# Optimization experiments

Hardware: AMD Instinct MI355X
Metric: run time of the kernel (lower is better)

The kernel has to match this reference:

```python
import jax, jax.numpy as jnp
import numpy as np

B, T, S, D = 32, 128, 2048, 1024


def setup_inputs() -> dict:
    key = jax.random.key(0)
    k1, k2, k3, k4 = jax.random.split(key, 4)
    source = jax.random.normal(k1, (B, T, D), dtype=jnp.float32)
    memory_bank = jax.random.normal(k2, (B, S, D), dtype=jnp.float32)
    # lengths in [1, S] so no query row is fully masked
    memory_lengths = jax.random.randint(k3, (B,), 1, S + 1, dtype=jnp.int64)
    # nn.Linear(2*dim, dim, bias=False) weight, torch layout [out, in]
    bound = 1.0 / np.sqrt(2 * D)
    W_out = jax.random.uniform(k4, (D, 2 * D), dtype=jnp.float32, minval=-bound, maxval=bound)
    return {"source": source, "memory_bank": memory_bank,
            "W_out": W_out, "memory_lengths": memory_lengths}


def reference(source, memory_bank, W_out, memory_lengths):
    # dot score: [B, T, S]
    align = jnp.einsum("btd,bsd->bts", source, memory_bank)
    # sequence mask from lengths: [B, S]
    mask = jnp.arange(S)[None, :] < memory_lengths[:, None]
    align = jnp.where(mask[:, None, :], align, -jnp.inf)
    align_vectors = jax.nn.softmax(align, axis=-1)            # [B, T, S]
    c = jnp.einsum("bts,bsd->btd", align_vectors, memory_bank)  # [B, T, D]
    concat_c = jnp.concatenate([c, source], axis=-1)            # [B, T, 2D]
    attn_h = jnp.tanh(concat_c @ W_out.T)                       # [B, T, D]
    # transpose to [T, B, ...] as original (one_step=False path)
    return attn_h.transpose(1, 0, 2), align_vectors.transpose(1, 0, 2)
```

## Files before the change

### kernel.cpp

```cpp
#include <hip/hip_runtime.h>
#include <hip/hip_bf16.h>
#include <stdint.h>

#define B_ 32
#define T_ 128
#define S_ 2048
#define D_ 1024

typedef float floatx4 __attribute__((ext_vector_type(4)));
typedef float f32x4 __attribute__((ext_vector_type(4)));
typedef unsigned short u16x4 __attribute__((ext_vector_type(4)));
typedef unsigned short u16x8 __attribute__((ext_vector_type(8)));
typedef __bf16 bf16x8 __attribute__((ext_vector_type(8)));

__device__ __forceinline__ unsigned short f2bf(float x){
  __hip_bfloat16 h = __float2bfloat16(x);
  return __builtin_bit_cast(unsigned short, h);
}
__device__ __forceinline__ float bf2f(unsigned short u){
  __hip_bfloat16 h = __builtin_bit_cast(__hip_bfloat16, u);
  return __bfloat162float(h);
}
__device__ __forceinline__ f32x4 mfma16(u16x8 a, u16x8 b, f32x4 c){
  return __builtin_amdgcn_mfma_f32_16x16x32_bf16(
      __builtin_bit_cast(bf16x8, a), __builtin_bit_cast(bf16x8, b), c, 0, 0, 0);
}

__global__ __launch_bounds__(512, 4) void k_align(
    const float* __restrict__ src, const float* __restrict__ mb,
    float* __restrict__ logits)
{
  __shared__ unsigned short SH[2][4][128][32];
  const int b = blockIdx.x, sblk = blockIdx.y;
  const int tid = threadIdx.x, lane = tid & 63, wave = tid >> 6;
  const int wr = wave >> 2, wc = wave & 3;
  const float* Ag = src + (size_t)b * T_ * D_;
  const float* Bg = mb + (size_t)b * S_ * D_ + (size_t)sblk * 128 * D_;

  f32x4 acc[4][2];
  #pragma unroll
  for (int m = 0; m < 4; m++)
    #pragma unroll
    for (int n = 0; n < 2; n++) acc[m][n] = (f32x4){0.f, 0.f, 0.f, 0.f};

  const int r0 = tid >> 3;
  const int c40 = (tid & 7) * 4;
  const int sw0 = ((((c40 >> 3) ^ ((r0 >> 1) & 3)) << 3) | (c40 & 7));
  const int r1 = r0 + 64;
  const int sw1 = ((((c40 >> 3) ^ ((r1 >> 1) & 3)) << 3) | (c40 & 7));

  floatx4 ra[2], rb[2];
  ra[0] = *(const floatx4*)(Ag + (size_t)r0 * D_ + c40);
  ra[1] = *(const floatx4*)(Ag + (size_t)r1 * D_ + c40);
  rb[0] = *(const floatx4*)(Bg + (size_t)r0 * D_ + c40);
  rb[1] = *(const floatx4*)(Bg + (size_t)r1 * D_ + c40);

  {
    u16x4 ah, al, bh, bl;
    #pragma unroll
    for (int i = 0; i < 4; i++) {
      unsigned short h = f2bf(ra[0][i]); float hf = bf2f(h);
      ah[i] = h; al[i] = f2bf(ra[0][i] - hf);
      h = f2bf(rb[0][i]); hf = bf2f(h);
      bh[i] = h; bl[i] = f2bf(rb[0][i] - hf);
    }
    *(u16x4*)&SH[0][0][r0][sw0] = ah;
    *(u16x4*)&SH[0][1][r0][sw0] = al;
    *(u16x4*)&SH[0][2][r0][sw0] = bh;
    *(u16x4*)&SH[0][3][r0][sw0] = bl;
    #pragma unroll
    for (int i = 0; i < 4; i++) {
      unsigned short h = f2bf(ra[1][i]); float hf = bf2f(h);
      ah[i] = h; al[i] = f2bf(ra[1][i] - hf);
      h = f2bf(rb[1][i]); hf = bf2f(h);
      bh[i] = h; bl[i] = f2bf(rb[1][i] - hf);
    }
    *(u16x4*)&SH[0][0][r1][sw1] = ah;
    *(u16x4*)&SH[0][1][r1][sw1] = al;
    *(u16x4*)&SH[0][2][r1][sw1] = bh;
    *(u16x4*)&SH[0][3][r1][sw1] = bl;
  }
  __syncthreads();

  for (int it = 0; it < 32; ++it) {
    const int cur = it & 1, nxt = cur ^ 1;
    const bool more = (it + 1 < 32);
    if (more) {
      const int k0 = (it + 1) * 32;
      ra[0] = *(const floatx4*)(Ag + (size_t)r0 * D_ + k0 + c40);
      ra[1] = *(const floatx4*)(Ag + (size_t)r1 * D_ + k0 + c40);
      rb[0] = *(const floatx4*)(Bg + (size_t)r0 * D_ + k0 + c40);
      rb[1] = *(const floatx4*)(Bg + (size_t)r1 * D_ + k0 + c40);
    }
    {
      const int kb = (lane >> 4) << 3;
      u16x8 a_h[4], a_l[4], b_h[2], b_l[2];
      #pragma unroll
      for (int m = 0; m < 4; m++) {
        int r = wr * 64 + m * 16 + (lane & 15);
        int kbs = (((kb >> 3) ^ ((r >> 1) & 3)) << 3);
        a_h[m] = *(const u16x8*)&SH[cur][0][r][kbs];
        a_l[m] = *(const u16x8*)&SH[cur][1][r][kbs];
      }
      #pragma unroll
      for (int n = 0; n < 2; n++) {
        int r = wc * 32 + n * 16 + (lane & 15);
        int kbs = (((kb >> 3) ^ ((r >> 1) & 3)) << 3);
        b_h[n] = *(const u16x8*)&SH[cur][2][r][kbs];
        b_l[n] = *(const u16x8*)&SH[cur][3][r][kbs];
      }
      #pragma unroll
      for (int m = 0; m < 4; m++)
        #pragma unroll
        for (int n = 0; n < 2; n++) {
          acc[m][n] = mfma16(a_h[m], b_h[n], acc[m][n]);
          acc[m][n] = mfma16(a_h[m], b_l[n], acc[m][n]);
          acc[m][n] = mfma16(a_l[m], b_h[n], acc[m][n]);
        }
    }
    if (more) {
      u16x4 ah, al, bh, bl;
      #pragma unroll
      for (int i = 0; i < 4; i++) {
        unsigned short h = f2bf(ra[0][i]); float hf = bf2f(h);
        ah[i] = h; al[i] = f2bf(ra[0][i] - hf);
        h = f2bf(rb[0][i]); hf = bf2f(h);
        bh[i] = h; bl[i] = f2bf(rb[0][i] - hf);
      }
      *(u16x4*)&SH[nxt][0][r0][sw0] = ah;
      *(u16x4*)&SH[nxt][1][r0][sw0] = al;
      *(u16x4*)&SH[nxt][2][r0][sw0] = bh;
      *(u16x4*)&SH[nxt][3][r0][sw0] = bl;
      #pragma unroll
      for (int i = 0; i < 4; i++) {
        unsigned short h = f2bf(ra[1][i]); float hf = bf2f(h);
        ah[i] = h; al[i] = f2bf(ra[1][i] - hf);
        h = f2bf(rb[1][i]); hf = bf2f(h);
        bh[i] = h; bl[i] = f2bf(rb[1][i] - hf);
      }
      *(u16x4*)&SH[nxt][0][r1][sw1] = ah;
      *(u16x4*)&SH[nxt][1][r1][sw1] = al;
      *(u16x4*)&SH[nxt][2][r1][sw1] = bh;
      *(u16x4*)&SH[nxt][3][r1][sw1] = bl;
    }
    __syncthreads();
  }

  #pragma unroll
  for (int m = 0; m < 4; m++)
    #pragma unroll
    for (int n = 0; n < 2; n++)
      #pragma unroll
      for (int j = 0; j < 4; j++) {
        int t = wr * 64 + m * 16 + ((lane >> 4) << 2) + j;
        int s = sblk * 128 + wc * 32 + n * 16 + (lane & 15);
        logits[((size_t)b * T_ + t) * S_ + s] = acc[m][n][j];
      }
}

__global__ __launch_bounds__(256) void k_softmax(
    const float* __restrict__ logits, const int* __restrict__ lens,
    float* __restrict__ out1, unsigned short* __restrict__ pbf)
{
  const int bt = blockIdx.x;
  const int b = bt >> 7, t = bt & 127;
  const int probe = lens[1];
  const int len = (probe == 0) ? lens[2 * b] : lens[b];
  const float* row = logits + (size_t)bt * S_;
  const int tid = threadIdx.x, lane = tid & 63, wave = tid >> 6;

  floatx4 v[2];
  float mx = -3.0e38f;
  #pragma unroll
  for (int j = 0; j < 2; j++) {
    int f4 = tid + 256 * j;
    v[j] = *(const floatx4*)(row + f4 * 4);
    #pragma unroll
    for (int i = 0; i < 4; i++) {
      int s = f4 * 4 + i;
      if (s < len) mx = fmaxf(mx, v[j][i]);
    }
  }
  #pragma unroll
  for (int off = 1; off < 64; off <<= 1) mx = fmaxf(mx, __shfl_xor(mx, off));
  __shared__ float red[8];
  if (lane == 0) red[wave] = mx;
  __syncthreads();
  mx = fmaxf(fmaxf(red[0], red[1]), fmaxf(red[2], red[3]));

  float sum = 0.f;
  floatx4 e[2];
  #pragma unroll
  for (int j = 0; j < 2; j++) {
    int f4 = tid + 256 * j;
    #pragma unroll
    for (int i = 0; i < 4; i++) {
      int s = f4 * 4 + i;
      float ee = (s < len) ? __expf(v[j][i] - mx) : 0.f;
      e[j][i] = ee; sum += ee;
    }
  }
  #pragma unroll
  for (int off = 1; off < 64; off <<= 1) sum += __shfl_xor(sum, off);
  if (lane == 0) red[4 + wave] = sum;
  __syncthreads();
  sum = red[4] + red[5] + red[6] + red[7];
  const float inv = 1.0f / sum;

  float* orow = out1 + ((size_t)t * B_ + b) * S_;
  unsigned short* prow = pbf + (size_t)bt * S_;
  #pragma unroll
  for (int j = 0; j < 2; j++) {
    int f4 = tid + 256 * j;
    floatx4 o;
    u16x4 pk;
    #pragma unroll
    for (int i = 0; i < 4; i++) { o[i] = e[j][i] * inv; pk[i] = f2bf(o[i]); }
    *(floatx4*)(orow + f4 * 4) = o;
    *(u16x4*)(prow + f4 * 4) = pk;
  }
}

__global__ __launch_bounds__(256, 2) void k_pv(
    const unsigned short* __restrict__ pbf, const float* __restrict__ mb,
    float* __restrict__ cout)
{
  __shared__ unsigned short As[128][72];
  __shared__ unsigned short BsT[64][72];
  const int b = blockIdx.x, dblk = blockIdx.y;
  const int tid = threadIdx.x, lane = tid & 63, wave = tid >> 6;
  const int wr = wave >> 1, wc = wave & 1;
  const unsigned short* Pg = pbf + (size_t)b * T_ * S_;
  const float* Bg = mb + (size_t)b * S_ * D_ + dblk * 64;

  f32x4 acc[4][2];
  #pragma unroll
  for (int m = 0; m < 4; m++)
    #pragma unroll
    for (int n = 0; n < 2; n++) acc[m][n] = (f32x4){0.f, 0.f, 0.f, 0.f};

  const int gs = tid & 15, gd = tid >> 4;
  const int s0 = gs * 4, d0 = gd * 4;

  u16x8 ra[4];
  floatx4 rb[4];
  #pragma unroll
  for (int j = 0; j < 4; j++) {
    int g = tid + 256 * j;
    int row = g >> 3, c8 = (g & 7) * 8;
    ra[j] = *(const u16x8*)(Pg + (size_t)row * S_ + c8);
  }
  #pragma unroll
  for (int j = 0; j < 4; j++)
    rb[j] = *(const floatx4*)(Bg + (size_t)(s0 + j) * D_ + d0);

  for (int k0 = 0; k0 < S_; k0 += 64) {
    #pragma unroll
    for (int j = 0; j < 4; j++) {
      int g = tid + 256 * j;
      int row = g >> 3, c8 = (g & 7) * 8;
      *(u16x8*)&As[row][c8] = ra[j];
    }
    #pragma unroll
    for (int jj = 0; jj < 4; jj++) {
      u16x4 w = { f2bf(rb[0][jj]), f2bf(rb[1][jj]), f2bf(rb[2][jj]), f2bf(rb[3][jj]) };
      *(u16x4*)&BsT[d0 + jj][s0] = w;
    }
    __syncthreads();
    if (k0 + 64 < S_) {
      #pragma unroll
      for (int j = 0; j < 4; j++) {
        int g = tid + 256 * j;
        int row = g >> 3, c8 = (g & 7) * 8;
        ra[j] = *(const u16x8*)(Pg + (size_t)row * S_ + (k0 + 64) + c8);
      }
      #pragma unroll
      for (int j = 0; j < 4; j++)
        rb[j] = *(const floatx4*)(Bg + (size_t)(k0 + 64 + s0 + j) * D_ + d0);
    }
    #pragma unroll
    for (int kk = 0; kk < 2; kk++) {
      int kb = kk * 32 + ((lane >> 4) << 3);
      u16x8 a[4], bb[2];
      #pragma unroll
      for (int m = 0; m < 4; m++)
        a[m] = *(const u16x8*)&As[wr * 64 + m * 16 + (lane & 15)][kb];
      #pragma unroll
      for (int n = 0; n < 2; n++)
        bb[n] = *(const u16x8*)&BsT[wc * 32 + n * 16 + (lane & 15)][kb];
      #pragma unroll
      for (int m = 0; m < 4; m++)
        #pragma unroll
        for (int n = 0; n < 2; n++)
          acc[m][n] = mfma16(a[m], bb[n], acc[m][n]);
    }
    __syncthreads();
  }
  #pragma unroll
  for (int m = 0; m < 4; m++)
    #pragma unroll
    for (int n = 0; n < 2; n++)
      #pragma unroll
      for (int j = 0; j < 4; j++) {
        int t = wr * 64 + m * 16 + ((lane >> 4) << 2) + j;
        int d = dblk * 64 + wc * 32 + n * 16 + (lane & 15);
        cout[((size_t)b * T_ + t) * D_ + d] = acc[m][n][j];
      }
}

__global__ __launch_bounds__(256, 2) void k_proj(
    const float* __restrict__ cbuf, const float* __restrict__ src,
    const float* __restrict__ w, float* __restrict__ out0)
{
  __shared__ unsigned short Ah[128][72];
  __shared__ unsigned short Bh[64][72];
  const int b = blockIdx.x, nblk = blockIdx.y;
  const int tid = threadIdx.x, lane = tid & 63, wave = tid >> 6;
  const int wr = wave >> 1, wc = wave & 1;
  const float* Ca = cbuf + (size_t)b * T_ * D_;
  const float* Sa = src + (size_t)b * T_ * D_;

  f32x4 acc[4][2];
  #pragma unroll
  for (int m = 0; m < 4; m++)
    #pragma unroll
    for (int n = 0; n < 2; n++) acc[m][n] = (f32x4){0.f, 0.f, 0.f, 0.f};

  floatx4 ra[8], rb[4];
  #pragma unroll
  for (int j = 0; j < 8; j++) {
    int f4 = tid + 256 * j;
    int row = f4 >> 4, c4 = (f4 & 15) * 4;
    ra[j] = *(const floatx4*)(Ca + (size_t)row * D_ + c4);
  }
  #pragma unroll
  for (int j = 0; j < 4; j++) {
    int f4 = tid + 256 * j;
    int row = f4 >> 4, c4 = (f4 & 15) * 4;
    rb[j] = *(const floatx4*)(w + (size_t)(nblk * 64 + row) * (2 * D_) + c4);
  }

  for (int k0 = 0; k0 < 2 * D_; k0 += 64) {
    #pragma unroll
    for (int j = 0; j < 8; j++) {
      int f4 = tid + 256 * j;
      int row = f4 >> 4, c4 = (f4 & 15) * 4;
      u16x4 ah;
      #pragma unroll
      for (int i = 0; i < 4; i++) ah[i] = f2bf(ra[j][i]);
      *(u16x4*)&Ah[row][c4] = ah;
    }
    #pragma unroll
    for (int j = 0; j < 4; j++) {
      int f4 = tid + 256 * j;
      int row = f4 >> 4, c4 = (f4 & 15) * 4;
      u16x4 bh;
      #pragma unroll
      for (int i = 0; i < 4; i++) bh[i] = f2bf(rb[j][i]);
      *(u16x4*)&Bh[row][c4] = bh;
    }
    __syncthreads();
    if (k0 + 64 < 2 * D_) {
      int kn = k0 + 64;
      const float* Asrc = (kn < D_) ? (Ca + kn) : (Sa + (kn - D_));
      #pragma unroll
      for (int j = 0; j < 8; j++) {
        int f4 = tid + 256 * j;
        int row = f4 >> 4, c4 = (f4 & 15) * 4;
        ra[j] = *(const floatx4*)(Asrc + (size_t)row * D_ + c4);
      }
      #pragma unroll
      for (int j = 0; j < 4; j++) {
        int f4 = tid + 256 * j;
        int row = f4 >> 4, c4 = (f4 & 15) * 4;
        rb[j] = *(const floatx4*)(w + (size_t)(nblk * 64 + row) * (2 * D_) + kn + c4);
      }
    }
    #pragma unroll
    for (int kk = 0; kk < 2; kk++) {
      int kb = kk * 32 + ((lane >> 4) << 3);
      u16x8 a[4], bb[2];
      #pragma unroll
      for (int m = 0; m < 4; m++)
        a[m] = *(const u16x8*)&Ah[wr * 64 + m * 16 + (lane & 15)][kb];
      #pragma unroll
      for (int n = 0; n < 2; n++)
        bb[n] = *(const u16x8*)&Bh[wc * 32 + n * 16 + (lane & 15)][kb];
      #pragma unroll
      for (int m = 0; m < 4; m++)
        #pragma unroll
        for (int n = 0; n < 2; n++)
          acc[m][n] = mfma16(a[m], bb[n], acc[m][n]);
    }
    __syncthreads();
  }
  #pragma unroll
  for (int m = 0; m < 4; m++)
    #pragma unroll
    for (int n = 0; n < 2; n++)
      #pragma unroll
      for (int j = 0; j < 4; j++) {
        int t = wr * 64 + m * 16 + ((lane >> 4) << 2) + j;
        int d = nblk * 64 + wc * 32 + n * 16 + (lane & 15);
        out0[(size_t)t * (B_ * D_) + (size_t)b * D_ + d] = tanhf(acc[m][n][j]);
      }
}

extern "C" void kernel_launch(void* const* d_in, const int* in_sizes, int n_in,
                              void* d_out, int out_size, void* d_ws, size_t ws_size,
                              hipStream_t stream) {
  const float* src = (const float*)d_in[0];
  const float* mb  = (const float*)d_in[1];
  const float* w   = (const float*)d_in[2];
  const int*   len = (const int*)d_in[3];

  float* out0 = (float*)d_out;
  float* out1 = out0 + (size_t)T_ * B_ * D_;

  float* logits = (float*)d_ws;
  float* cbuf   = logits + (size_t)B_ * T_ * S_;
  unsigned short* pbf =
      (unsigned short*)(cbuf + (size_t)B_ * T_ * D_);

  k_align  <<<dim3(B_, S_ / 128), 512, 0, stream>>>(src, mb, logits);
  k_softmax<<<dim3(B_ * T_),      256, 0, stream>>>(logits, len, out1, pbf);
  k_pv     <<<dim3(B_, D_ / 64),  256, 0, stream>>>(pbf, mb, cbuf);
  k_proj   <<<dim3(B_, D_ / 64),  256, 0, stream>>>(cbuf, src, w, out0);
}
```

Baseline: 211.8 us.

## Split align GEMM over K into two partial buffers, reduced in softmax

The align kernel's grid gets a third dimension that splits the D reduction into two halves. Each half writes its partial logits to a separate workspace buffer, and the softmax kernel adds the two partials as it loads them. The shared-memory double buffer is replaced by a single buffer with an extra barrier, which lowers LDS use per block. The aim is more blocks, more occupancy and more latency hiding, at the cost of doubling logits write and read traffic and giving up the load/compute overlap the double buffer provided.

```diff
diff --git a/kernel.cpp b/kernel.cpp
--- a/kernel.cpp
+++ b/kernel.cpp
@@ -28,14 +28,15 @@
 
 __global__ __launch_bounds__(512, 4) void k_align(
     const float* __restrict__ src, const float* __restrict__ mb,
-    float* __restrict__ logits)
+    float* __restrict__ lpart)
 {
-  __shared__ unsigned short SH[2][4][128][32];
-  const int b = blockIdx.x, sblk = blockIdx.y;
+  __shared__ unsigned short Ah[128][32], Al[128][32], Bh[128][32], Bl[128][32];
+  const int b = blockIdx.x, sblk = blockIdx.y, z = blockIdx.z;
+  const int kbase = z * (D_ / 2);
   const int tid = threadIdx.x, lane = tid & 63, wave = tid >> 6;
   const int wr = wave >> 2, wc = wave & 3;
-  const float* Ag = src + (size_t)b * T_ * D_;
-  const float* Bg = mb + (size_t)b * S_ * D_ + (size_t)sblk * 128 * D_;
+  const float* Ag = src + (size_t)b * T_ * D_ + kbase;
+  const float* Bg = mb + (size_t)b * S_ * D_ + (size_t)sblk * 128 * D_ + kbase;
 
   f32x4 acc[4][2];
   #pragma unroll
@@ -55,42 +56,39 @@
   rb[0] = *(const floatx4*)(Bg + (size_t)r0 * D_ + c40);
   rb[1] = *(const floatx4*)(Bg + (size_t)r1 * D_ + c40);
 
-  {
-    u16x4 ah, al, bh, bl;
-    #pragma unroll
-    for (int i = 0; i < 4; i++) {
-      unsigned short h = f2bf(ra[0][i]); float hf = bf2f(h);
-      ah[i] = h; al[i] = f2bf(ra[0][i] - hf);
-      h = f2bf(rb[0][i]); hf = bf2f(h);
-      bh[i] = h; bl[i] = f2bf(rb[0][i] - hf);
-    }
-    *(u16x4*)&SH[0][0][r0][sw0] = ah;
-    *(u16x4*)&SH[0][1][r0][sw0] = al;
-    *(u16x4*)&SH[0][2][r0][sw0] = bh;
-    *(u16x4*)&SH[0][3][r0][sw0] = bl;
-    #pragma unroll
-    for (int i = 0; i < 4; i++) {
-      unsigned short h = f2bf(ra[1][i]); float hf = bf2f(h);
-      ah[i] = h; al[i] = f2bf(ra[1][i] - hf);
-      h = f2bf(rb[1][i]); hf = bf2f(h);
-      bh[i] = h; bl[i] = f2bf(rb[1][i] - hf);
-    }
-    *(u16x4*)&SH[0][0][r1][sw1] = ah;
-    *(u16x4*)&SH[0][1][r1][sw1] = al;
-    *(u16x4*)&SH[0][2][r1][sw1] = bh;
-    *(u16x4*)&SH[0][3][r1][sw1] = bl;
-  }
-  __syncthreads();
-
-  for (int it = 0; it < 32; ++it) {
-    const int cur = it & 1, nxt = cur ^ 1;
-    const bool more = (it + 1 < 32);
-    if (more) {
-      const int k0 = (it + 1) * 32;
-      ra[0] = *(const floatx4*)(Ag + (size_t)r0 * D_ + k0 + c40);
-      ra[1] = *(const floatx4*)(Ag + (size_t)r1 * D_ + k0 + c40);
-      rb[0] = *(const floatx4*)(Bg + (size_t)r0 * D_ + k0 + c40);
-      rb[1] = *(const floatx4*)(Bg + (size_t)r1 * D_ + k0 + c40);
+  for (int k0 = 0; k0 < D_ / 2; k0 += 32) {
+    {
+      u16x4 ah, al, bh, bl;
+      #pragma unroll
+      for (int i = 0; i < 4; i++) {
+        unsigned short h = f2bf(ra[0][i]); float hf = bf2f(h);
+        ah[i] = h; al[i] = f2bf(ra[0][i] - hf);
+        h = f2bf(rb[0][i]); hf = bf2f(h);
+        bh[i] = h; bl[i] = f2bf(rb[0][i] - hf);
+      }
+      *(u16x4*)&Ah[r0][sw0] = ah;
+      *(u16x4*)&Al[r0][sw0] = al;
+      *(u16x4*)&Bh[r0][sw0] = bh;
+      *(u16x4*)&Bl[r0][sw0] = bl;
+      #pragma unroll
+      for (int i = 0; i < 4; i++) {
+        unsigned short h = f2bf(ra[1][i]); float hf = bf2f(h);
+        ah[i] = h; al[i] = f2bf(ra[1][i] - hf);
+        h = f2bf(rb[1][i]); hf = bf2f(h);
+        bh[i] = h; bl[i] = f2bf(rb[1][i] - hf);
+      }
+      *(u16x4*)&Ah[r1][sw1] = ah;
+      *(u16x4*)&Al[r1][sw1] = al;
+      *(u16x4*)&Bh[r1][sw1] = bh;
+      *(u16x4*)&Bl[r1][sw1] = bl;
+    }
+    __syncthreads();
+    if (k0 + 32 < D_ / 2) {
+      const int kn = k0 + 32;
+      ra[0] = *(const floatx4*)(Ag + (size_t)r0 * D_ + kn + c40);
+      ra[1] = *(const floatx4*)(Ag + (size_t)r1 * D_ + kn + c40);
+      rb[0] = *(const floatx4*)(Bg + (size_t)r0 * D_ + kn + c40);
+      rb[1] = *(const floatx4*)(Bg + (size_t)r1 * D_ + kn + c40);
     }
     {
       const int kb = (lane >> 4) << 3;
@@ -99,15 +97,15 @@
       for (int m = 0; m < 4; m++) {
         int r = wr * 64 + m * 16 + (lane & 15);
         int kbs = (((kb >> 3) ^ ((r >> 1) & 3)) << 3);
-        a_h[m] = *(const u16x8*)&SH[cur][0][r][kbs];
-        a_l[m] = *(const u16x8*)&SH[cur][1][r][kbs];
+        a_h[m] = *(const u16x8*)&Ah[r][kbs];
+        a_l[m] = *(const u16x8*)&Al[r][kbs];
       }
       #pragma unroll
       for (int n = 0; n < 2; n++) {
         int r = wc * 32 + n * 16 + (lane & 15);
         int kbs = (((kb >> 3) ^ ((r >> 1) & 3)) << 3);
-        b_h[n] = *(const u16x8*)&SH[cur][2][r][kbs];
-        b_l[n] = *(const u16x8*)&SH[cur][3][r][kbs];
+        b_h[n] = *(const u16x8*)&Bh[r][kbs];
+        b_l[n] = *(const u16x8*)&Bl[r][kbs];
       }
       #pragma unroll
       for (int m = 0; m < 4; m++)
@@ -118,34 +116,9 @@
           acc[m][n] = mfma16(a_l[m], b_h[n], acc[m][n]);
         }
     }
-    if (more) {
-      u16x4 ah, al, bh, bl;
-      #pragma unroll
-      for (int i = 0; i < 4; i++) {
-        unsigned short h = f2bf(ra[0][i]); float hf = bf2f(h);
-        ah[i] = h; al[i] = f2bf(ra[0][i] - hf);
-        h = f2bf(rb[0][i]); hf = bf2f(h);
-        bh[i] = h; bl[i] = f2bf(rb[0][i] - hf);
-      }
-      *(u16x4*)&SH[nxt][0][r0][sw0] = ah;
-      *(u16x4*)&SH[nxt][1][r0][sw0] = al;
-      *(u16x4*)&SH[nxt][2][r0][sw0] = bh;
-      *(u16x4*)&SH[nxt][3][r0][sw0] = bl;
-      #pragma unroll
-      for (int i = 0; i < 4; i++) {
-        unsigned short h = f2bf(ra[1][i]); float hf = bf2f(h);
-        ah[i] = h; al[i] = f2bf(ra[1][i] - hf);
-        h = f2bf(rb[1][i]); hf = bf2f(h);
-        bh[i] = h; bl[i] = f2bf(rb[1][i] - hf);
-      }
-      *(u16x4*)&SH[nxt][0][r1][sw1] = ah;
-      *(u16x4*)&SH[nxt][1][r1][sw1] = al;
-      *(u16x4*)&SH[nxt][2][r1][sw1] = bh;
-      *(u16x4*)&SH[nxt][3][r1][sw1] = bl;
-    }
-    __syncthreads();
-  }
-
+    __syncthreads();
+  }
+  float* lz = lpart + (size_t)z * B_ * T_ * S_;
   #pragma unroll
   for (int m = 0; m < 4; m++)
     #pragma unroll
@@ -154,19 +127,20 @@
       for (int j = 0; j < 4; j++) {
         int t = wr * 64 + m * 16 + ((lane >> 4) << 2) + j;
         int s = sblk * 128 + wc * 32 + n * 16 + (lane & 15);
-        logits[((size_t)b * T_ + t) * S_ + s] = acc[m][n][j];
+        lz[((size_t)b * T_ + t) * S_ + s] = acc[m][n][j];
       }
 }
 
 __global__ __launch_bounds__(256) void k_softmax(
-    const float* __restrict__ logits, const int* __restrict__ lens,
+    const float* __restrict__ lpart, const int* __restrict__ lens,
     float* __restrict__ out1, unsigned short* __restrict__ pbf)
 {
   const int bt = blockIdx.x;
   const int b = bt >> 7, t = bt & 127;
   const int probe = lens[1];
   const int len = (probe == 0) ? lens[2 * b] : lens[b];
-  const float* row = logits + (size_t)bt * S_;
+  const float* row0 = lpart + (size_t)bt * S_;
+  const float* row1 = row0 + (size_t)B_ * T_ * S_;
   const int tid = threadIdx.x, lane = tid & 63, wave = tid >> 6;
 
   floatx4 v[2];
@@ -174,7 +148,10 @@
   #pragma unroll
   for (int j = 0; j < 2; j++) {
     int f4 = tid + 256 * j;
-    v[j] = *(const floatx4*)(row + f4 * 4);
+    floatx4 v0 = *(const floatx4*)(row0 + f4 * 4);
+    floatx4 v1 = *(const floatx4*)(row1 + f4 * 4);
+    #pragma unroll
+    for (int i = 0; i < 4; i++) v[j][i] = v0[i] + v1[i];
     #pragma unroll
     for (int i = 0; i < 4; i++) {
       int s = f4 * 4 + i;
@@ -417,13 +394,13 @@
   float* out0 = (float*)d_out;
   float* out1 = out0 + (size_t)T_ * B_ * D_;
 
-  float* logits = (float*)d_ws;
-  float* cbuf   = logits + (size_t)B_ * T_ * S_;
+  float* lpart = (float*)d_ws;
+  float* cbuf  = lpart + 2 * (size_t)B_ * T_ * S_;
   unsigned short* pbf =
       (unsigned short*)(cbuf + (size_t)B_ * T_ * D_);
 
-  k_align  <<<dim3(B_, S_ / 128), 512, 0, stream>>>(src, mb, logits);
-  k_softmax<<<dim3(B_ * T_),      256, 0, stream>>>(logits, len, out1, pbf);
-  k_pv     <<<dim3(B_, D_ / 64),  256, 0, stream>>>(pbf, mb, cbuf);
-  k_proj   <<<dim3(B_, D_ / 64),  256, 0, stream>>>(cbuf, src, w, out0);
-}
+  k_align  <<<dim3(B_, S_ / 128, 2), 512, 0, stream>>>(src, mb, lpart);
+  k_softmax<<<dim3(B_ * T_),         256, 0, stream>>>(lpart, len, out1, pbf);
+  k_pv     <<<dim3(B_, D_ / 64),     256, 0, stream>>>(pbf, mb, cbuf);
+  k_proj   <<<dim3(B_, D_ / 64),     256, 0, stream>>>(cbuf, src, w, out0);
+}
```

After: 225.9 us. 1.07x slower.
